# Optimization experiments

Hardware: AMD Instinct MI355X
Metric: run time of the kernel (lower is better)

Reference implementation:

```python
import jax, jax.numpy as jnp
import numpy as np

N_NODES = 50000


def _gcn_norm(edge_index, num_nodes):
    """PyG GCNConv normalization: add self-loops, symmetric deg^{-1/2} weights."""
    loops = jnp.arange(num_nodes, dtype=edge_index.dtype)
    src = jnp.concatenate([edge_index[0], loops])
    dst = jnp.concatenate([edge_index[1], loops])
    deg = jax.ops.segment_sum(jnp.ones_like(dst, dtype=jnp.float32), dst,
                              num_segments=num_nodes)
    dinv = jax.lax.rsqrt(jnp.maximum(deg, 1.0))  # self-loops guarantee deg>=1
    norm = dinv[src] * dinv[dst]                 # [E + N]
    return src, dst, norm


def _gcn_conv(x, W, b, src, dst, norm, num_nodes):
    h = x @ W                                    # [N, out] dense GEMM
    msg = h[src] * norm[:, None]                 # gather + scale
    agg = jax.ops.segment_sum(msg, dst, num_segments=num_nodes)
    return agg + b


def setup_inputs() -> dict:
    key = jax.random.key(0)
    ks = jax.random.split(key, 8)
    d = 128
    scale = 1.0 / np.sqrt(d)
    emb = jax.random.normal(ks[0], (N_NODES, d), dtype=jnp.float32)
    W1 = jax.random.normal(ks[1], (d, d), dtype=jnp.float32) * scale
    W2 = jax.random.normal(ks[2], (d, d), dtype=jnp.float32) * scale
    W3 = jax.random.normal(ks[3], (d, d), dtype=jnp.float32) * scale
    b1 = jnp.zeros((d,), dtype=jnp.float32)
    b2 = jnp.zeros((d,), dtype=jnp.float32)
    b3 = jnp.zeros((d,), dtype=jnp.float32)
    edge_index = jax.random.randint(ks[4], (2, 600000), 0, N_NODES, dtype=jnp.int64)
    return {"emb": emb, "W1": W1, "b1": b1, "W2": W2, "b2": b2,
            "W3": W3, "b3": b3, "edge_index": edge_index}


def reference(emb, W1, b1, W2, b2, W3, b3, edge_index):
    # Eval-mode forward: F.dropout(training=False) is identity.
    src, dst, norm = _gcn_norm(edge_index, N_NODES)
    x = emb
    x = jax.nn.relu(_gcn_conv(x, W1, b1, src, dst, norm, N_NODES))
    x = jax.nn.relu(_gcn_conv(x, W2, b2, src, dst, norm, N_NODES))
    x = _gcn_conv(x, W3, b3, src, dst, norm, N_NODES)
    x = x.at[0].set(0.0)  # x[0] = zeros(x.shape[1])
    return x
```

## Files before the change

kernel.cpp:

```cpp
#include <hip/hip_runtime.h>
#include <hip/hip_fp16.h>

#define NN 50000
#define D 128
#define STRIDE 64

typedef __attribute__((ext_vector_type(16))) float f32x16;
typedef _Float16 h16;
typedef __attribute__((ext_vector_type(8))) _Float16 h16x8;

struct alignas(16) H8 { h16 h[8]; };

typedef const __attribute__((address_space(1))) void gvoid;
typedef __attribute__((address_space(3))) void lvoid;

__global__ __launch_bounds__(256) void wprep_kernel(const float* __restrict__ W1,
                                                    const float* __restrict__ W2,
                                                    const float* __restrict__ W3,
                                                    h16* __restrict__ Wsp,
                                                    int* __restrict__ cnt) {
    const int b  = blockIdx.x;
    const int w  = b >> 3;
    const int ks = b & 7;
    const float* W = w == 0 ? W1 : (w == 1 ? W2 : W3);
    h16* dst = Wsp + w * 32768;
    const int l  = threadIdx.x & 63;
    const int ct = threadIdx.x >> 6;
    const int n  = ct * 32 + (l & 31);
    const int lh = l >> 5;
    const int kbase = ks * 16 + lh * 8;
    H8 hi8, lo8;
#pragma unroll
    for (int j = 0; j < 8; j++) {
        float wv = W[(kbase + j) * D + n];
        h16 hi = (h16)wv;
        hi8.h[j] = hi;
        lo8.h[j] = (h16)(wv - (float)hi);
    }
    const int base = ((ks * 4 + ct) * 64 + l) * 8;
    *(H8*)(dst + base)         = hi8;
    *(H8*)(dst + base + 16384) = lo8;
    for (int i = b * 256 + threadIdx.x; i < NN; i += 24 * 256) cnt[i] = 0;
}

__global__ __launch_bounds__(256, 2) void gemm_mfma(const void* __restrict__ Xv, int x_is_f32,
                                                    const h16* __restrict__ Wsp,
                                                    h16* __restrict__ H, int M,
                                                    const int* __restrict__ srcA,
                                                    const int* __restrict__ dstA,
                                                    int* __restrict__ cnt,
                                                    int* __restrict__ slots, int noct) {
    __shared__ h16 Ws[32768];
    {
        const int t = threadIdx.x;
#pragma unroll
        for (int i = 0; i < 16; i++) {
            const int off = (i * 256 + t) * 8;
            __builtin_amdgcn_global_load_lds((gvoid*)(Wsp + off), (lvoid*)(Ws + off),
                                             16, 0, 0);
        }
    }

    if (srcA) {
        int t = blockIdx.x * 256 + threadIdx.x;
        if (t < noct) {
            int4 sa = ((const int4*)srcA)[2 * t];
            int4 sb = ((const int4*)srcA)[2 * t + 1];
            int4 da = ((const int4*)dstA)[2 * t];
            int4 db = ((const int4*)dstA)[2 * t + 1];
            int p0 = atomicAdd(&cnt[da.x], 1);
            int p1 = atomicAdd(&cnt[da.y], 1);
            int p2 = atomicAdd(&cnt[da.z], 1);
            int p3 = atomicAdd(&cnt[da.w], 1);
            int p4 = atomicAdd(&cnt[db.x], 1);
            int p5 = atomicAdd(&cnt[db.y], 1);
            int p6 = atomicAdd(&cnt[db.z], 1);
            int p7 = atomicAdd(&cnt[db.w], 1);
            if (p0 < STRIDE - 4) slots[da.x * STRIDE + p0] = sa.x;
            if (p1 < STRIDE - 4) slots[da.y * STRIDE + p1] = sa.y;
            if (p2 < STRIDE - 4) slots[da.z * STRIDE + p2] = sa.z;
            if (p3 < STRIDE - 4) slots[da.w * STRIDE + p3] = sa.w;
            if (p4 < STRIDE - 4) slots[db.x * STRIDE + p4] = sb.x;
            if (p5 < STRIDE - 4) slots[db.y * STRIDE + p5] = sb.y;
            if (p6 < STRIDE - 4) slots[db.z * STRIDE + p6] = sb.z;
            if (p7 < STRIDE - 4) slots[db.w * STRIDE + p7] = sb.w;
        }
    }

    __syncthreads();

    const int wave = threadIdx.x >> 6;
    const int lane = threadIdx.x & 63;
    const int row0 = blockIdx.x * 128 + wave * 32;
    const int arow = min(row0 + (lane & 31), M - 1);
    const int koff = (lane >> 5) * 8;

    f32x16 acc[4] = {};

#pragma unroll
    for (int ks = 0; ks < 8; ks++) {
        h16x8 ahi, alo;
        if (x_is_f32) {
            const float* p = (const float*)Xv + (size_t)arow * D + koff + ks * 16;
            float4 fa = *(const float4*)p;
            float4 fb = *(const float4*)(p + 4);
            float f[8] = {fa.x, fa.y, fa.z, fa.w, fb.x, fb.y, fb.z, fb.w};
#pragma unroll
            for (int j = 0; j < 8; j++) {
                h16 hi = (h16)f[j];
                ahi[j] = hi;
                alo[j] = (h16)(f[j] - (float)hi);
            }
        } else {
            const h16* p = (const h16*)Xv + (size_t)arow * D + koff + ks * 16;
            ahi = *(const h16x8*)p;
        }
#pragma unroll
        for (int ct = 0; ct < 4; ct++) {
            const int base = ((ks * 4 + ct) * 64 + lane) * 8;
            h16x8 bhi = *(const h16x8*)(Ws + base);
            h16x8 blo = *(const h16x8*)(Ws + base + 16384);
            acc[ct] = __builtin_amdgcn_mfma_f32_32x32x16_f16(ahi, bhi, acc[ct], 0, 0, 0);
            acc[ct] = __builtin_amdgcn_mfma_f32_32x32x16_f16(ahi, blo, acc[ct], 0, 0, 0);
            if (x_is_f32)
                acc[ct] = __builtin_amdgcn_mfma_f32_32x32x16_f16(alo, bhi, acc[ct], 0, 0, 0);
        }
    }

    __syncthreads();
    {
        h16* C_lds = Ws;
        const int col0 = lane & 31;
        const int lr0  = 4 * (lane >> 5);
#pragma unroll
        for (int ct = 0; ct < 4; ct++) {
#pragma unroll
            for (int r = 0; r < 16; r++) {
                const int lrow = lr0 + (r & 3) + 8 * (r >> 2);
                C_lds[(wave * 32 + lrow) * D + ct * 32 + col0] = (h16)acc[ct][r];
            }
        }
        const h16* src = C_lds + wave * 32 * D;
        h16* gdst = H + (size_t)row0 * D;
#pragma unroll
        for (int j = 0; j < 8; j++) {
            const int i = j * 64 + lane;
            const int row = row0 + (i >> 4);
            if (row < M)
                *(h16x8*)(gdst + (size_t)i * 8) = *(const h16x8*)(src + i * 8);
        }
    }
}

__global__ __launch_bounds__(256) void agg_kernel(const h16* __restrict__ H,
                                                  const int* __restrict__ cnt,
                                                  const int* __restrict__ slots,
                                                  const float* __restrict__ bias,
                                                  h16* __restrict__ out16,
                                                  float* __restrict__ out32,
                                                  int mode) {
    const int lane  = threadIdx.x & 63;
    const int q     = lane >> 4;
    const int col   = (lane & 15) * 8;
    const int node0 = blockIdx.x * 16 + (threadIdx.x >> 6) * 4;

    const float4 bb0 = *(const float4*)(bias + col);
    const float4 bb1 = *(const float4*)(bias + col + 4);

    for (int nn = 0; nn < 4; nn++) {
        const int node = node0 + nn;
        const int c = __builtin_amdgcn_readfirstlane(cnt[node]);
        const float di = rsqrtf((float)c + 1.0f);
        const int sbase = node * STRIDE;
        const int pc = min((c + 8) & ~7, STRIDE);

        float aA[8] = {0.f, 0.f, 0.f, 0.f, 0.f, 0.f, 0.f, 0.f};
        float aB[8] = {0.f, 0.f, 0.f, 0.f, 0.f, 0.f, 0.f, 0.f};

        int sa = slots[sbase + q];
        int sb = slots[sbase + 4 + q];

        for (int p = 0; p < pc; p += 8) {
            int sa_n = slots[sbase + min(p + 8 + q, STRIDE - 1)];
            int sb_n = slots[sbase + min(p + 12 + q, STRIDE - 1)];
            const int ja = p + q;
            const int jb = p + 4 + q;
            const int ca = (ja < c) ? sa : node;
            const int cb = (jb < c) ? sb : node;
            float wa = (ja < c) ? rsqrtf((float)cnt[ca] + 1.0f) : ((ja == c) ? di : 0.f);
            float wb = (jb < c) ? rsqrtf((float)cnt[cb] + 1.0f) : ((jb == c) ? di : 0.f);
            h16x8 va = *(const h16x8*)(H + (size_t)ca * D + col);
            h16x8 vb = *(const h16x8*)(H + (size_t)cb * D + col);
#pragma unroll
            for (int j = 0; j < 8; j++) {
                aA[j] = fmaf(wa, (float)va[j], aA[j]);
                aB[j] = fmaf(wb, (float)vb[j], aB[j]);
            }
            sa = sa_n; sb = sb_n;
        }

#pragma unroll
        for (int j = 0; j < 8; j++) {
            float v = aA[j] + aB[j];
            v += __shfl_xor(v, 16, 64);
            v += __shfl_xor(v, 32, 64);
            aA[j] = v;
        }

        if (lane < 16) {
            float r[8];
            r[0] = fmaf(di, aA[0], bb0.x); r[1] = fmaf(di, aA[1], bb0.y);
            r[2] = fmaf(di, aA[2], bb0.z); r[3] = fmaf(di, aA[3], bb0.w);
            r[4] = fmaf(di, aA[4], bb1.x); r[5] = fmaf(di, aA[5], bb1.y);
            r[6] = fmaf(di, aA[6], bb1.z); r[7] = fmaf(di, aA[7], bb1.w);
            if (mode == 0) {
                h16x8 o;
#pragma unroll
                for (int j = 0; j < 8; j++) o[j] = (h16)fmaxf(r[j], 0.f);
                *(h16x8*)(out16 + (size_t)node * D + col) = o;
            } else {
                if (node == 0) {
#pragma unroll
                    for (int j = 0; j < 8; j++) r[j] = 0.f;
                }
                *(float4*)(out32 + (size_t)node * D + col)     = make_float4(r[0], r[1], r[2], r[3]);
                *(float4*)(out32 + (size_t)node * D + col + 4) = make_float4(r[4], r[5], r[6], r[7]);
            }
        }
    }
}


extern "C" void kernel_launch(void* const* d_in, const int* in_sizes, int n_in,
                              void* d_out, int out_size, void* d_ws, size_t ws_size,
                              hipStream_t stream) {
    const float* emb = (const float*)d_in[0];
    const float* W1  = (const float*)d_in[1];
    const float* b1  = (const float*)d_in[2];
    const float* W2  = (const float*)d_in[3];
    const float* b2  = (const float*)d_in[4];
    const float* W3  = (const float*)d_in[5];
    const float* b3  = (const float*)d_in[6];
    const int*   ei  = (const int*)d_in[7];

    const int E = in_sizes[7] / 2;
    const int* srcA = ei;
    const int* dstA = ei + E;
    float* out = (float*)d_out;

    char* ws = (char*)d_ws;
    size_t off = 0;
    auto alloc = [&](size_t bytes) -> void* {
        void* p = ws + off;
        off = (off + bytes + 255) & ~(size_t)255;
        return p;
    };
    h16* h      = (h16*)alloc((size_t)NN * D * 2);
    h16* x16    = (h16*)alloc((size_t)NN * D * 2);
    int* cnt    = (int*)alloc((size_t)NN * 4);
    int* slots  = (int*)alloc((size_t)NN * STRIDE * 4);
    h16* Wsp    = (h16*)alloc((size_t)3 * 32768 * 2);

    const int gemm_grid = (NN + 127) / 128;
    const int agg_grid  = NN / 16;
    const int noct = E / 8;

    wprep_kernel<<<24, 256, 0, stream>>>(W1, W2, W3, Wsp, cnt);
    gemm_mfma<<<gemm_grid, 256, 0, stream>>>(emb, 1, Wsp, h, NN,
                                             srcA, dstA, cnt, slots, noct);
    agg_kernel<<<agg_grid, 256, 0, stream>>>(h, cnt, slots, b1, x16, nullptr, 0);
    gemm_mfma<<<gemm_grid, 256, 0, stream>>>(x16, 0, Wsp + 32768, h, NN,
                                             nullptr, nullptr, nullptr, nullptr, 0);
    agg_kernel<<<agg_grid, 256, 0, stream>>>(h, cnt, slots, b2, x16, nullptr, 0);
    gemm_mfma<<<gemm_grid, 256, 0, stream>>>(x16, 0, Wsp + 65536, h, NN,
                                             nullptr, nullptr, nullptr, nullptr, 0);
    agg_kernel<<<agg_grid, 256, 0, stream>>>(h, cnt, slots, b3, nullptr, out, 1);
}
```

Measured before the change: 253.0 us.

## Split edge bucketing out of GEMM and read weights from global instead of LDS

The CSR-style slot fill (atomics on per-destination counters) moves out of the first GEMM into its own kernel launched after it. The GEMM no longer stages the 64 KB weight split into LDS; each lane reads its B fragments straight from global memory, relying on the cache. LDS is cut to a 32 KB output staging buffer and launch bounds rise to 4 blocks per SM for more occupancy. The trade-off is an extra launch, repeated global/L2 weight fetches per wave, and the atomic fill no longer overlapping the GEMM.

```diff
diff --git a/kernel.cpp b/kernel.cpp
--- a/kernel.cpp
+++ b/kernel.cpp
@@ -10,9 +10,6 @@
 typedef __attribute__((ext_vector_type(8))) _Float16 h16x8;
 
 struct alignas(16) H8 { h16 h[8]; };
-
-typedef const __attribute__((address_space(1))) void gvoid;
-typedef __attribute__((address_space(3))) void lvoid;
 
 __global__ __launch_bounds__(256) void wprep_kernel(const float* __restrict__ W1,
                                                     const float* __restrict__ W2,
@@ -43,57 +40,45 @@
     for (int i = b * 256 + threadIdx.x; i < NN; i += 24 * 256) cnt[i] = 0;
 }
 
-__global__ __launch_bounds__(256, 2) void gemm_mfma(const void* __restrict__ Xv, int x_is_f32,
+__global__ __launch_bounds__(256) void fill_kernel(const int* __restrict__ srcA,
+                                                   const int* __restrict__ dstA,
+                                                   int* __restrict__ cnt,
+                                                   int* __restrict__ slots, int noct) {
+    int t = blockIdx.x * 256 + threadIdx.x;
+    if (t >= noct) return;
+    int4 sa = ((const int4*)srcA)[2 * t];
+    int4 sb = ((const int4*)srcA)[2 * t + 1];
+    int4 da = ((const int4*)dstA)[2 * t];
+    int4 db = ((const int4*)dstA)[2 * t + 1];
+    int p0 = atomicAdd(&cnt[da.x], 1);
+    int p1 = atomicAdd(&cnt[da.y], 1);
+    int p2 = atomicAdd(&cnt[da.z], 1);
+    int p3 = atomicAdd(&cnt[da.w], 1);
+    int p4 = atomicAdd(&cnt[db.x], 1);
+    int p5 = atomicAdd(&cnt[db.y], 1);
+    int p6 = atomicAdd(&cnt[db.z], 1);
+    int p7 = atomicAdd(&cnt[db.w], 1);
+    if (p0 < STRIDE - 4) slots[da.x * STRIDE + p0] = sa.x;
+    if (p1 < STRIDE - 4) slots[da.y * STRIDE + p1] = sa.y;
+    if (p2 < STRIDE - 4) slots[da.z * STRIDE + p2] = sa.z;
+    if (p3 < STRIDE - 4) slots[da.w * STRIDE + p3] = sa.w;
+    if (p4 < STRIDE - 4) slots[db.x * STRIDE + p4] = sb.x;
+    if (p5 < STRIDE - 4) slots[db.y * STRIDE + p5] = sb.y;
+    if (p6 < STRIDE - 4) slots[db.z * STRIDE + p6] = sb.z;
+    if (p7 < STRIDE - 4) slots[db.w * STRIDE + p7] = sb.w;
+}
+
+__global__ __launch_bounds__(256, 4) void gemm_mfma(const void* __restrict__ Xv, int x_is_f32,
                                                     const h16* __restrict__ Wsp,
-                                                    h16* __restrict__ H, int M,
-                                                    const int* __restrict__ srcA,
-                                                    const int* __restrict__ dstA,
-                                                    int* __restrict__ cnt,
-                                                    int* __restrict__ slots, int noct) {
-    __shared__ h16 Ws[32768];
-    {
-        const int t = threadIdx.x;
-#pragma unroll
-        for (int i = 0; i < 16; i++) {
-            const int off = (i * 256 + t) * 8;
-            __builtin_amdgcn_global_load_lds((gvoid*)(Wsp + off), (lvoid*)(Ws + off),
-                                             16, 0, 0);
-        }
-    }
-
-    if (srcA) {
-        int t = blockIdx.x * 256 + threadIdx.x;
-        if (t < noct) {
-            int4 sa = ((const int4*)srcA)[2 * t];
-            int4 sb = ((const int4*)srcA)[2 * t + 1];
-            int4 da = ((const int4*)dstA)[2 * t];
-            int4 db = ((const int4*)dstA)[2 * t + 1];
-            int p0 = atomicAdd(&cnt[da.x], 1);
-            int p1 = atomicAdd(&cnt[da.y], 1);
-            int p2 = atomicAdd(&cnt[da.z], 1);
-            int p3 = atomicAdd(&cnt[da.w], 1);
-            int p4 = atomicAdd(&cnt[db.x], 1);
-            int p5 = atomicAdd(&cnt[db.y], 1);
-            int p6 = atomicAdd(&cnt[db.z], 1);
-            int p7 = atomicAdd(&cnt[db.w], 1);
-            if (p0 < STRIDE - 4) slots[da.x * STRIDE + p0] = sa.x;
-            if (p1 < STRIDE - 4) slots[da.y * STRIDE + p1] = sa.y;
-            if (p2 < STRIDE - 4) slots[da.z * STRIDE + p2] = sa.z;
-            if (p3 < STRIDE - 4) slots[da.w * STRIDE + p3] = sa.w;
-            if (p4 < STRIDE - 4) slots[db.x * STRIDE + p4] = sb.x;
-            if (p5 < STRIDE - 4) slots[db.y * STRIDE + p5] = sb.y;
-            if (p6 < STRIDE - 4) slots[db.z * STRIDE + p6] = sb.z;
-            if (p7 < STRIDE - 4) slots[db.w * STRIDE + p7] = sb.w;
-        }
-    }
-
-    __syncthreads();
+                                                    h16* __restrict__ H, int M) {
+    __shared__ h16 Cs[16384];
 
     const int wave = threadIdx.x >> 6;
     const int lane = threadIdx.x & 63;
     const int row0 = blockIdx.x * 128 + wave * 32;
     const int arow = min(row0 + (lane & 31), M - 1);
     const int koff = (lane >> 5) * 8;
+    const h16* Wl = Wsp + lane * 8;
 
     f32x16 acc[4] = {};
 
@@ -117,9 +102,9 @@
         }
 #pragma unroll
         for (int ct = 0; ct < 4; ct++) {
-            const int base = ((ks * 4 + ct) * 64 + lane) * 8;
-            h16x8 bhi = *(const h16x8*)(Ws + base);
-            h16x8 blo = *(const h16x8*)(Ws + base + 16384);
+            const int fo = ((ks * 4 + ct) * 64) * 8;
+            h16x8 bhi = *(const h16x8*)(Wl + fo);
+            h16x8 blo = *(const h16x8*)(Wl + fo + 16384);
             acc[ct] = __builtin_amdgcn_mfma_f32_32x32x16_f16(ahi, bhi, acc[ct], 0, 0, 0);
             acc[ct] = __builtin_amdgcn_mfma_f32_32x32x16_f16(ahi, blo, acc[ct], 0, 0, 0);
             if (x_is_f32)
@@ -127,9 +112,7 @@
         }
     }
 
-    __syncthreads();
     {
-        h16* C_lds = Ws;
         const int col0 = lane & 31;
         const int lr0  = 4 * (lane >> 5);
 #pragma unroll
@@ -137,10 +120,10 @@
 #pragma unroll
             for (int r = 0; r < 16; r++) {
                 const int lrow = lr0 + (r & 3) + 8 * (r >> 2);
-                C_lds[(wave * 32 + lrow) * D + ct * 32 + col0] = (h16)acc[ct][r];
-            }
-        }
-        const h16* src = C_lds + wave * 32 * D;
+                Cs[(wave * 32 + lrow) * D + ct * 32 + col0] = (h16)acc[ct][r];
+            }
+        }
+        const h16* src = Cs + wave * 32 * D;
         h16* gdst = H + (size_t)row0 * D;
 #pragma unroll
         for (int j = 0; j < 8; j++) {
@@ -266,13 +249,11 @@
     const int noct = E / 8;
 
     wprep_kernel<<<24, 256, 0, stream>>>(W1, W2, W3, Wsp, cnt);
-    gemm_mfma<<<gemm_grid, 256, 0, stream>>>(emb, 1, Wsp, h, NN,
-                                             srcA, dstA, cnt, slots, noct);
+    gemm_mfma<<<gemm_grid, 256, 0, stream>>>(emb, 1, Wsp, h, NN);
+    fill_kernel<<<(noct + 255) / 256, 256, 0, stream>>>(srcA, dstA, cnt, slots, noct);
     agg_kernel<<<agg_grid, 256, 0, stream>>>(h, cnt, slots, b1, x16, nullptr, 0);
-    gemm_mfma<<<gemm_grid, 256, 0, stream>>>(x16, 0, Wsp + 32768, h, NN,
-                                             nullptr, nullptr, nullptr, nullptr, 0);
+    gemm_mfma<<<gemm_grid, 256, 0, stream>>>(x16, 0, Wsp + 32768, h, NN);
     agg_kernel<<<agg_grid, 256, 0, stream>>>(h, cnt, slots, b2, x16, nullptr, 0);
-    gemm_mfma<<<gemm_grid, 256, 0, stream>>>(x16, 0, Wsp + 65536, h, NN,
-                                             nullptr, nullptr, nullptr, nullptr, 0);
+    gemm_mfma<<<gemm_grid, 256, 0, stream>>>(x16, 0, Wsp + 65536, h, NN);
     agg_kernel<<<agg_grid, 256, 0, stream>>>(h, cnt, slots, b3, nullptr, out, 1);
 }
```

Result: slower. 272.5 us (+7.7%).
